# Kernel optimization log

Measured on AMD Instinct MI355X. Metric: run time of the kernel, lower is better.

Reference implementation:

```python
import jax, jax.numpy as jnp
import numpy as np

LN_EPS = 1e-5  # torch.nn.LayerNorm default


def setup_inputs() -> dict:
    key = jax.random.key(0)
    k1, k2 = jax.random.split(key)
    N, D_IN, D_OUT, G = 4096, 512, 512, 32
    x = jax.random.normal(k1, (N, D_IN), dtype=jnp.float32)
    ln_w = jnp.ones((D_IN,), dtype=jnp.float32)
    ln_b = jnp.zeros((D_IN,), dtype=jnp.float32)
    scale = 1.0 / (np.sqrt(D_IN) * np.sqrt(G))
    fouriercoeffs = jax.random.normal(k2, (2, D_OUT, D_IN, G), dtype=jnp.float32) * scale
    bias = jnp.zeros((1, D_OUT), dtype=jnp.float32)
    return {"x": x, "ln_w": ln_w, "ln_b": ln_b, "fouriercoeffs": fouriercoeffs, "bias": bias}


def reference(x, ln_w, ln_b, fouriercoeffs, bias):
    # LayerNorm over last dim
    mu = jnp.mean(x, axis=-1, keepdims=True)
    var = jnp.mean((x - mu) ** 2, axis=-1, keepdims=True)
    xn = (x - mu) * jax.lax.rsqrt(var + LN_EPS) * ln_w + ln_b
    G = fouriercoeffs.shape[-1]
    k = jnp.arange(1, G + 1, dtype=xn.dtype)           # [G]
    arg = xn[:, :, None] * k                            # [N, D_in, G]
    c = jnp.cos(arg)
    s = jnp.sin(arg)
    # contraction over (inputdim, gridsize) -> GEMM-shaped einsum
    y = jnp.einsum('big,oig->bo', c, fouriercoeffs[0])
    y = y + jnp.einsum('big,oig->bo', s, fouriercoeffs[1])
    y = y + bias
    return y
```

## Files before the change

### kernel.cpp

```cpp
#include <hip/hip_runtime.h>
#include <hip/hip_bf16.h>


#define N_ROWS 4096
#define D_IN   512
#define D_OUT  512
#define KT     16384
#define BM 128
#define BN 128
#define SPLITK 4

typedef short short8 __attribute__((ext_vector_type(8)));
typedef float float4v __attribute__((ext_vector_type(4)));

__device__ inline unsigned int pack2bf(float a, float b) {
    __hip_bfloat162 h = __float22bfloat162_rn(make_float2(a, b));
    union { __hip_bfloat162 h; unsigned int u; } cv;
    cv.h = h;
    return cv.u;
}

__device__ inline unsigned short bf16_1(float a) {
    union { float f; unsigned int u; } cv;
    cv.f = a;
    unsigned int r = (cv.u + 0x7fff + ((cv.u >> 16) & 1)) >> 16;
    return (unsigned short)r;
}

__global__ __launch_bounds__(256) void ln_stats(const float* __restrict__ x,
        float2* __restrict__ mu_rs) {
    const int t = threadIdx.x;
    const int row = blockIdx.x * 4 + (t >> 6);
    const int lane = t & 63;
    const float4* xr = (const float4*)(x + (size_t)row * D_IN);
    float4 a = xr[lane];
    float4 c = xr[lane + 64];
    float s = a.x + a.y + a.z + a.w + c.x + c.y + c.z + c.w;
    float q = a.x * a.x + a.y * a.y + a.z * a.z + a.w * a.w
            + c.x * c.x + c.y * c.y + c.z * c.z + c.w * c.w;
    #pragma unroll
    for (int off = 32; off > 0; off >>= 1) {
        s += __shfl_down(s, off, 64);
        q += __shfl_down(q, off, 64);
    }
    if (lane == 0) {
        float mu = s * (1.f / D_IN);
        float var = q * (1.f / D_IN) - mu * mu;
        mu_rs[row] = make_float2(mu, rsqrtf(var + 1e-5f));
    }
}

__global__ __launch_bounds__(256) void feat_seed(const float* __restrict__ x,
        const float* __restrict__ w, const float* __restrict__ b,
        const float2* __restrict__ mu_rs, float2* __restrict__ csT) {
    __shared__ float2 tile[64][65];
    const int t = threadIdx.x;
    const int r0 = blockIdx.x * 64, i0 = blockIdx.y * 64;
    const int rr = t >> 6;
    const int cc = t & 63;
    const float wv = w[i0 + cc], bv = b[i0 + cc];
    #pragma unroll
    for (int p = 0; p < 16; ++p) {
        const int row = r0 + p * 4 + rr;
        float v = x[(size_t)row * D_IN + i0 + cc];
        float2 mr = mu_rs[row];
        float xn = (v - mr.x) * mr.y * wv + bv;
        float sn, cn;
        __sincosf(xn, &sn, &cn);
        tile[p * 4 + rr][cc] = make_float2(cn, sn);
    }
    __syncthreads();
    #pragma unroll
    for (int p = 0; p < 16; ++p) {
        const int dim = p * 4 + rr;
        csT[(size_t)(i0 + dim) * N_ROWS + r0 + cc] = tile[cc][dim];
    }
}

__global__ __launch_bounds__(256) void cvt_kernel(const float* __restrict__ fc,
        unsigned short* __restrict__ Wb) {
    size_t e = ((size_t)blockIdx.x * 256 + threadIdx.x) * 8;
    const float4* in = (const float4*)(fc + e);
    float4 a = in[0];
    float4 c = in[1];
    uint4 o;
    o.x = pack2bf(a.x, a.y);
    o.y = pack2bf(a.z, a.w);
    o.z = pack2bf(c.x, c.y);
    o.w = pack2bf(c.z, c.w);
    *(uint4*)(Wb + e) = o;
}

__device__ inline void stage_feats(unsigned short* Abuf, float2 cs, int ttype,
                                   int frow, int ihalf) {
    const float c1 = cs.x, s1 = cs.y;
    const float c2 = c1 + c1;
    float prev = ttype ? 0.f : 1.f;
    float cur  = ttype ? s1 : c1;
    const int rbase = frow * 64;
    const int sw = frow & 7;
    unsigned int us[4];
    #pragma unroll
    for (int d = 0; d < 16; ++d) {
        float f0 = cur;
        float f1 = __builtin_fmaf(c2, cur, -prev);
        float f2 = __builtin_fmaf(c2, f1, -cur);
        prev = f1;
        cur = f2;
        us[d & 3] = pack2bf(f0, f1);
        if ((d & 3) == 3) {
            const int kc = ihalf * 4 + (d >> 2);
            *(uint4*)&Abuf[rbase + ((kc ^ sw) << 3)] =
                make_uint4(us[0], us[1], us[2], us[3]);
        }
    }
}

__device__ inline void gl_lds16(const unsigned short* gsrc, unsigned short* ldst) {
    __builtin_amdgcn_global_load_lds(
        (const __attribute__((address_space(1))) unsigned int*)gsrc,
        (__attribute__((address_space(3))) unsigned int*)ldst, 16, 0, 0);
}

__device__ inline void read_af(const unsigned short* As, short8 (&af)[2][4],
                               int wm, int lm, int lq, int swA) {
    #pragma unroll
    for (int h = 0; h < 2; ++h)
        #pragma unroll
        for (int tm = 0; tm < 4; ++tm)
            af[h][tm] = *(const short8*)
                &As[(wm + tm * 16 + lm) * 64 + (((h * 4 + lq) ^ swA) << 3)];
}

__device__ inline void read_bf(const unsigned short* Bp, short8 (&bf)[2][4],
                               int bBase) {
    #pragma unroll
    for (int h = 0; h < 2; ++h)
        #pragma unroll
        for (int tn = 0; tn < 4; ++tn)
            bf[h][tn] = *(const short8*)&Bp[bBase + tn * 1024 + h * 256];
}

__device__ inline void mfma_block(short8 (&af)[2][4], short8 (&bf)[2][4],
                                  float4v (&acc)[4][4]) {
    __builtin_amdgcn_s_setprio(1);
    #pragma unroll
    for (int h = 0; h < 2; ++h)
        #pragma unroll
        for (int tm = 0; tm < 4; ++tm)
            #pragma unroll
            for (int tn = 0; tn < 4; ++tn)
                acc[tm][tn] = __builtin_amdgcn_mfma_f32_16x16x32_bf16(
                    af[h][tm], bf[h][tn], acc[tm][tn], 0, 0, 0);
    __builtin_amdgcn_s_setprio(0);
}

__global__ __launch_bounds__(256, 2) void fkan_gemm(const float2* __restrict__ csT,
        const unsigned short* __restrict__ Wb, unsigned short* __restrict__ pb) {
    __shared__ unsigned short As[2][BM * 64];
    __shared__ unsigned short Bs[3][BN * 64];
    const int t = threadIdx.x;
    const int row0 = blockIdx.x * BM;
    const int col0 = blockIdx.y * BN;
    const int kz = blockIdx.z;
    const int k0 = kz * 4096;
    const int i0 = kz * 128;
    const int frow = t & 127;
    const int ihalf = t >> 7;
    const int l = t & 63, wv = t >> 6;
    const int wm = (wv & 1) * 64, wn = (wv >> 1) * 64;
    const int lm = l & 15, lq = l >> 4;
    const int c8 = l & 7, s8 = l >> 3;
    const unsigned short* Bg0 = Wb + (size_t)(col0 + wv * 32 + c8) * KT + k0 + s8 * 8;
    const int swA = lm & 7;
    const int bBase = ((wn >> 3) + (lm >> 3)) * 512 + lq * 64 + (lm & 7) * 8;

    const float2* csBase = csT + (size_t)(i0 + ihalf) * N_ROWS + row0 + frow;

    float4v acc[4][4];
    #pragma unroll
    for (int i = 0; i < 4; ++i)
        #pragma unroll
        for (int j = 0; j < 4; ++j)
            acc[i][j] = (float4v){0.f, 0.f, 0.f, 0.f};

    #pragma unroll
    for (int j = 0; j < 4; ++j)
        gl_lds16(Bg0 + (size_t)(j * 8) * KT, &Bs[0][(wv * 4 + j) * 512]);
    #pragma unroll
    for (int j = 0; j < 4; ++j)
        gl_lds16(Bg0 + 64 + (size_t)(j * 8) * KT, &Bs[1][(wv * 4 + j) * 512]);
    float2 c0 = csBase[0];
    float2 csA = csBase[2 * N_ROWS];
    stage_feats(&As[0][0], c0, 0, frow, ihalf);
    asm volatile("s_waitcnt vmcnt(4) lgkmcnt(0)" ::: "memory");
    __builtin_amdgcn_s_barrier();

    int rd = 0, wr = 2;
    for (int it = 0; it < 126; ++it) {
        const int p = it & 1;
        const unsigned short* Bp = &Bs[0][0] + rd * (BN * 64);
        {
            const int in = it + 2;
            const unsigned short* gb =
                Bg0 + (size_t)(in >> 6) * D_OUT * KT + (in & 63) * 64;
            unsigned short* ldst = &Bs[0][0] + wr * (BN * 64) + (wv * 4) * 512;
            #pragma unroll
            for (int j = 0; j < 4; ++j)
                gl_lds16(gb + (size_t)(j * 8) * KT, ldst + j * 512);
        }
        float2 csN = csBase[(size_t)(((it + 2) & 63) * 2) * N_ROWS];
        short8 af[2][4];
        read_af(&As[p][0], af, wm, lm, lq, swA);
        short8 bf[2][4];
        read_bf(Bp, bf, bBase);
        stage_feats(&As[p ^ 1][0], csA, (it + 1) >> 6, frow, ihalf);
        csA = csN;
        mfma_block(af, bf, acc);
        asm volatile("s_waitcnt vmcnt(5) lgkmcnt(0)" ::: "memory");
        __builtin_amdgcn_s_barrier();
        rd = (rd == 2) ? 0 : rd + 1;
        wr = (wr == 2) ? 0 : wr + 1;
    }
    {
        const unsigned short* Bp = &Bs[0][0];
        short8 af[2][4];
        read_af(&As[0][0], af, wm, lm, lq, swA);
        short8 bf[2][4];
        read_bf(Bp, bf, bBase);
        stage_feats(&As[1][0], csA, 1, frow, ihalf);
        mfma_block(af, bf, acc);
        asm volatile("s_waitcnt vmcnt(0) lgkmcnt(0)" ::: "memory");
        __builtin_amdgcn_s_barrier();
    }
    {
        const unsigned short* Bp = &Bs[1][0];
        short8 af[2][4];
        read_af(&As[1][0], af, wm, lm, lq, swA);
        short8 bf[2][4];
        read_bf(Bp, bf, bBase);
        mfma_block(af, bf, acc);
    }
    unsigned short* pc = pb + (size_t)kz * N_ROWS * D_OUT;
    #pragma unroll
    for (int tm = 0; tm < 4; ++tm)
        #pragma unroll
        for (int tn = 0; tn < 4; ++tn)
            #pragma unroll
            for (int r = 0; r < 4; ++r) {
                const int row = row0 + wm + tm * 16 + lq * 4 + r;
                const int col = col0 + wn + tn * 16 + lm;
                pc[(size_t)row * D_OUT + col] = bf16_1(acc[tm][tn][r]);
            }
}

__global__ __launch_bounds__(256) void reduce_kernel(const unsigned short* __restrict__ pb,
        const float* __restrict__ bias, float* __restrict__ out) {
    const size_t e = ((size_t)blockIdx.x * 256 + threadIdx.x) * 4;
    const int col = (int)(e & (D_OUT - 1));
    float4 s = *(const float4*)(bias + col);
    #pragma unroll
    for (int c = 0; c < SPLITK; ++c) {
        ushort4 u = *(const ushort4*)(pb + (size_t)c * N_ROWS * D_OUT + e);
        union { unsigned int u; float f; } f0, f1, f2, f3;
        f0.u = (unsigned int)u.x << 16;
        f1.u = (unsigned int)u.y << 16;
        f2.u = (unsigned int)u.z << 16;
        f3.u = (unsigned int)u.w << 16;
        s.x += f0.f; s.y += f1.f; s.z += f2.f; s.w += f3.f;
    }
    *(float4*)(out + e) = s;
}

extern "C" void kernel_launch(void* const* d_in, const int* in_sizes, int n_in,
                              void* d_out, int out_size, void* d_ws, size_t ws_size,
                              hipStream_t stream) {
    const float* x    = (const float*)d_in[0];
    const float* ln_w = (const float*)d_in[1];
    const float* ln_b = (const float*)d_in[2];
    const float* fc   = (const float*)d_in[3];
    const float* bias = (const float*)d_in[4];
    float* out = (float*)d_out;

    float2* csT = (float2*)d_ws;
    float2* mu_rs = (float2*)((char*)d_ws + (16u << 20));
    unsigned short* Wb = (unsigned short*)((char*)d_ws + (17u << 20));
    unsigned short* pbp = (unsigned short*)((char*)d_ws + (51u << 20));

    ln_stats<<<N_ROWS / 4, 256, 0, stream>>>(x, mu_rs);
    feat_seed<<<dim3(N_ROWS / 64, D_IN / 64), 256, 0, stream>>>(x, ln_w, ln_b, mu_rs, csT);
    cvt_kernel<<<8192, 256, 0, stream>>>(fc, Wb);
    fkan_gemm<<<dim3(N_ROWS / BM, D_OUT / BN, SPLITK), 256, 0, stream>>>(csT, Wb, pbp);
    reduce_kernel<<<2048, 256, 0, stream>>>(pbp, bias, out);
}
```

Before: 283.9 us.

## Generate Fourier A-fragments in registers and fuse preprocessing into one kernel

Merges the LayerNorm-stats, feature-seed and weight-conversion kernels into a single pre_kernel. That kernel also precomputes cos/sin at frequencies 1 and 16 as float4 seeds. The GEMM drops its A tile in LDS: each lane builds its bf16 A fragments directly in registers from the seeds with the Chebyshev recurrence, which removes LDS writes and reads and a barrier dependency. This adds per-lane recurrence work and duplicated seed loads from global, and the fused pre-kernel runs the weight conversion on only 256 blocks, which may lower its parallelism.

```diff
diff --git a/kernel.cpp b/kernel.cpp
--- a/kernel.cpp
+++ b/kernel.cpp
@@ -27,91 +27,66 @@
     return (unsigned short)r;
 }
 
-__global__ __launch_bounds__(256) void ln_stats(const float* __restrict__ x,
-        float2* __restrict__ mu_rs) {
+__global__ __launch_bounds__(256) void pre_kernel(const float* __restrict__ x,
+        const float* __restrict__ lnw, const float* __restrict__ lnb,
+        const float* __restrict__ fc, float4* __restrict__ csT2,
+        unsigned short* __restrict__ Wb) {
+    __shared__ __align__(16) float xs[16 * 516];
+    __shared__ float2 murs[16];
     const int t = threadIdx.x;
-    const int row = blockIdx.x * 4 + (t >> 6);
-    const int lane = t & 63;
-    const float4* xr = (const float4*)(x + (size_t)row * D_IN);
-    float4 a = xr[lane];
-    float4 c = xr[lane + 64];
-    float s = a.x + a.y + a.z + a.w + c.x + c.y + c.z + c.w;
-    float q = a.x * a.x + a.y * a.y + a.z * a.z + a.w * a.w
-            + c.x * c.x + c.y * c.y + c.z * c.z + c.w * c.w;
-    #pragma unroll
-    for (int off = 32; off > 0; off >>= 1) {
-        s += __shfl_down(s, off, 64);
-        q += __shfl_down(q, off, 64);
-    }
-    if (lane == 0) {
-        float mu = s * (1.f / D_IN);
-        float var = q * (1.f / D_IN) - mu * mu;
-        mu_rs[row] = make_float2(mu, rsqrtf(var + 1e-5f));
-    }
-}
-
-__global__ __launch_bounds__(256) void feat_seed(const float* __restrict__ x,
-        const float* __restrict__ w, const float* __restrict__ b,
-        const float2* __restrict__ mu_rs, float2* __restrict__ csT) {
-    __shared__ float2 tile[64][65];
-    const int t = threadIdx.x;
-    const int r0 = blockIdx.x * 64, i0 = blockIdx.y * 64;
-    const int rr = t >> 6;
-    const int cc = t & 63;
-    const float wv = w[i0 + cc], bv = b[i0 + cc];
-    #pragma unroll
-    for (int p = 0; p < 16; ++p) {
-        const int row = r0 + p * 4 + rr;
-        float v = x[(size_t)row * D_IN + i0 + cc];
-        float2 mr = mu_rs[row];
-        float xn = (v - mr.x) * mr.y * wv + bv;
-        float sn, cn;
-        __sincosf(xn, &sn, &cn);
-        tile[p * 4 + rr][cc] = make_float2(cn, sn);
+    const int r0 = blockIdx.x * 16;
+    {
+        const int row = t >> 4, tq = t & 15;
+        const float* xr = x + (size_t)(r0 + row) * D_IN;
+        float s = 0.f, q = 0.f;
+        #pragma unroll
+        for (int k = 0; k < 8; ++k) {
+            float4 v = *(const float4*)(xr + tq * 4 + k * 64);
+            *(float4*)&xs[row * 516 + tq * 4 + k * 64] = v;
+            s += v.x + v.y + v.z + v.w;
+            q += v.x * v.x + v.y * v.y + v.z * v.z + v.w * v.w;
+        }
+        #pragma unroll
+        for (int off = 8; off > 0; off >>= 1) {
+            s += __shfl_xor(s, off, 16);
+            q += __shfl_xor(q, off, 16);
+        }
+        if (tq == 0) {
+            float mu = s * (1.f / D_IN);
+            float var = q * (1.f / D_IN) - mu * mu;
+            murs[row] = make_float2(mu, rsqrtf(var + 1e-5f));
+        }
     }
     __syncthreads();
-    #pragma unroll
-    for (int p = 0; p < 16; ++p) {
-        const int dim = p * 4 + rr;
-        csT[(size_t)(i0 + dim) * N_ROWS + r0 + cc] = tile[cc][dim];
-    }
-}
-
-__global__ __launch_bounds__(256) void cvt_kernel(const float* __restrict__ fc,
-        unsigned short* __restrict__ Wb) {
-    size_t e = ((size_t)blockIdx.x * 256 + threadIdx.x) * 8;
-    const float4* in = (const float4*)(fc + e);
-    float4 a = in[0];
-    float4 c = in[1];
-    uint4 o;
-    o.x = pack2bf(a.x, a.y);
-    o.y = pack2bf(a.z, a.w);
-    o.z = pack2bf(c.x, c.y);
-    o.w = pack2bf(c.z, c.w);
-    *(uint4*)(Wb + e) = o;
-}
-
-__device__ inline void stage_feats(unsigned short* Abuf, float2 cs, int ttype,
-                                   int frow, int ihalf) {
-    const float c1 = cs.x, s1 = cs.y;
-    const float c2 = c1 + c1;
-    float prev = ttype ? 0.f : 1.f;
-    float cur  = ttype ? s1 : c1;
-    const int rbase = frow * 64;
-    const int sw = frow & 7;
-    unsigned int us[4];
-    #pragma unroll
-    for (int d = 0; d < 16; ++d) {
-        float f0 = cur;
-        float f1 = __builtin_fmaf(c2, cur, -prev);
-        float f2 = __builtin_fmaf(c2, f1, -cur);
-        prev = f1;
-        cur = f2;
-        us[d & 3] = pack2bf(f0, f1);
-        if ((d & 3) == 3) {
-            const int kc = ihalf * 4 + (d >> 2);
-            *(uint4*)&Abuf[rbase + ((kc ^ sw) << 3)] =
-                make_uint4(us[0], us[1], us[2], us[3]);
+    {
+        const int brow = t & 15, dimg = t >> 4;
+        const float2 mr = murs[brow];
+        #pragma unroll 4
+        for (int j = 0; j < 32; ++j) {
+            const int dim = j * 16 + dimg;
+            float xv = xs[brow * 516 + dim];
+            float xn = (xv - mr.x) * mr.y * lnw[dim] + lnb[dim];
+            float s1, c1;
+            __sincosf(xn, &s1, &c1);
+            float k2, c2, s2, c4, s4, c8, s8, c16, s16;
+            k2 = c1 + c1; c2  = __builtin_fmaf(k2, c1, -1.f); s2  = k2 * s1;
+            k2 = c2 + c2; c4  = __builtin_fmaf(k2, c2, -1.f); s4  = k2 * s2;
+            k2 = c4 + c4; c8  = __builtin_fmaf(k2, c4, -1.f); s8  = k2 * s4;
+            k2 = c8 + c8; c16 = __builtin_fmaf(k2, c8, -1.f); s16 = k2 * s8;
+            csT2[(size_t)dim * N_ROWS + r0 + brow] = make_float4(c1, s1, c16, s16);
+        }
+    }
+    {
+        size_t e = ((size_t)blockIdx.x * 256 + t) * 8;
+        for (int it2 = 0; it2 < 32; ++it2, e += (size_t)256 * 256 * 8) {
+            const float4* in = (const float4*)(fc + e);
+            float4 a = in[0], c = in[1];
+            uint4 o;
+            o.x = pack2bf(a.x, a.y);
+            o.y = pack2bf(a.z, a.w);
+            o.z = pack2bf(c.x, c.y);
+            o.w = pack2bf(c.z, c.w);
+            *(uint4*)(Wb + e) = o;
         }
     }
 }
@@ -122,42 +97,86 @@
         (__attribute__((address_space(3))) unsigned int*)ldst, 16, 0, 0);
 }
 
-__device__ inline void read_af(const unsigned short* As, short8 (&af)[2][4],
-                               int wm, int lm, int lq, int swA) {
-    #pragma unroll
-    for (int h = 0; h < 2; ++h)
+template<bool SIN>
+__device__ __forceinline__ void make_af(float4 sd, bool oddlq,
+                                        short8& a0, short8& a1) {
+    const float c1 = sd.x, s1 = sd.y, c16 = sd.z, s16 = sd.w;
+    const float k2 = c1 + c1;
+    float prev, cur;
+    if (SIN) {
+        float tt = s16 * c1;
+        float s17 = __builtin_fmaf(c16, s1, tt);
+        prev = oddlq ? s16 : 0.f;
+        cur  = oddlq ? s17 : s1;
+    } else {
+        float tt = s16 * s1;
+        float c17 = __builtin_fmaf(c16, c1, -tt);
+        prev = oddlq ? c16 : 1.f;
+        cur  = oddlq ? c17 : c1;
+    }
+    union { unsigned int u[8]; short8 s8v[2]; } U;
+    float p = prev, c = cur;
+    #pragma unroll
+    for (int d = 0; d < 8; ++d) {
+        float n1 = __builtin_fmaf(k2, c, -p);
+        U.u[d] = pack2bf(c, n1);
+        float n2 = __builtin_fmaf(k2, n1, -c);
+        p = n1;
+        c = n2;
+    }
+    a0 = U.s8v[0];
+    a1 = U.s8v[1];
+}
+
+template<bool SIN, bool PF, bool LDSEED>
+__device__ __forceinline__ void gemm_step(int it, int rd, int wr,
+        unsigned short (*Bs)[BN * 64], const unsigned short* Bg0, int wv,
+        const float4* const (&sb)[4], float4 (&sdU)[4], float4 (&sdL)[4],
+        int bBase, bool oddlq, float4v (&acc)[4][4]) {
+    if (PF) {
+        const int in = it + 2;
+        const unsigned short* gb =
+            Bg0 + (size_t)(in >> 6) * D_OUT * KT + (in & 63) * 64;
+        unsigned short* ldst = &Bs[wr][(wv * 4) * 512];
+        #pragma unroll
+        for (int j = 0; j < 4; ++j)
+            gl_lds16(gb + (size_t)(j * 8) * KT, ldst + j * 512);
+    }
+    if (LDSEED) {
         #pragma unroll
         for (int tm = 0; tm < 4; ++tm)
-            af[h][tm] = *(const short8*)
-                &As[(wm + tm * 16 + lm) * 64 + (((h * 4 + lq) ^ swA) << 3)];
-}
-
-__device__ inline void read_bf(const unsigned short* Bp, short8 (&bf)[2][4],
-                               int bBase) {
-    #pragma unroll
-    for (int h = 0; h < 2; ++h)
+            sdL[tm] = sb[tm][(size_t)((it + 1) & 63) * 8192];
+    }
+    const unsigned short* Bp = Bs[rd];
+    short8 bf0[4], bf1[4];
+    #pragma unroll
+    for (int tn = 0; tn < 4; ++tn) {
+        bf0[tn] = *(const short8*)&Bp[bBase + tn * 1024];
+        bf1[tn] = *(const short8*)&Bp[bBase + tn * 1024 + 64];
+    }
+    __builtin_amdgcn_s_setprio(1);
+    #pragma unroll
+    for (int tm = 0; tm < 4; ++tm) {
+        short8 a0, a1;
+        make_af<SIN>(sdU[tm], oddlq, a0, a1);
         #pragma unroll
         for (int tn = 0; tn < 4; ++tn)
-            bf[h][tn] = *(const short8*)&Bp[bBase + tn * 1024 + h * 256];
-}
-
-__device__ inline void mfma_block(short8 (&af)[2][4], short8 (&bf)[2][4],
-                                  float4v (&acc)[4][4]) {
-    __builtin_amdgcn_s_setprio(1);
-    #pragma unroll
-    for (int h = 0; h < 2; ++h)
-        #pragma unroll
-        for (int tm = 0; tm < 4; ++tm)
-            #pragma unroll
-            for (int tn = 0; tn < 4; ++tn)
-                acc[tm][tn] = __builtin_amdgcn_mfma_f32_16x16x32_bf16(
-                    af[h][tm], bf[h][tn], acc[tm][tn], 0, 0, 0);
+            acc[tm][tn] = __builtin_amdgcn_mfma_f32_16x16x32_bf16(
+                a0, bf0[tn], acc[tm][tn], 0, 0, 0);
+        #pragma unroll
+        for (int tn = 0; tn < 4; ++tn)
+            acc[tm][tn] = __builtin_amdgcn_mfma_f32_16x16x32_bf16(
+                a1, bf1[tn], acc[tm][tn], 0, 0, 0);
+    }
     __builtin_amdgcn_s_setprio(0);
 }
 
-__global__ __launch_bounds__(256, 2) void fkan_gemm(const float2* __restrict__ csT,
+#define FENCE8() do { asm volatile("s_waitcnt vmcnt(8)" ::: "memory"); \
+                      __builtin_amdgcn_s_barrier(); } while (0)
+#define ROT(v) (v) = ((v) == 2) ? 0 : (v) + 1
+
+__global__ __launch_bounds__(256, 2) void fkan_gemm(const float4* __restrict__ csT2,
         const unsigned short* __restrict__ Wb, unsigned short* __restrict__ pb) {
-    __shared__ unsigned short As[2][BM * 64];
     __shared__ unsigned short Bs[3][BN * 64];
     const int t = threadIdx.x;
     const int row0 = blockIdx.x * BM;
@@ -165,17 +184,19 @@
     const int kz = blockIdx.z;
     const int k0 = kz * 4096;
     const int i0 = kz * 128;
-    const int frow = t & 127;
-    const int ihalf = t >> 7;
     const int l = t & 63, wv = t >> 6;
     const int wm = (wv & 1) * 64, wn = (wv >> 1) * 64;
     const int lm = l & 15, lq = l >> 4;
+    const bool oddlq = (lq & 1) != 0;
     const int c8 = l & 7, s8 = l >> 3;
     const unsigned short* Bg0 = Wb + (size_t)(col0 + wv * 32 + c8) * KT + k0 + s8 * 8;
-    const int swA = lm & 7;
-    const int bBase = ((wn >> 3) + (lm >> 3)) * 512 + lq * 64 + (lm & 7) * 8;
-
-    const float2* csBase = csT + (size_t)(i0 + ihalf) * N_ROWS + row0 + frow;
+    const int bBase = ((wn >> 3) + (lm >> 3)) * 512
+                    + ((lq >> 1) * 4 + (lq & 1) * 2) * 64 + (lm & 7) * 8;
+    const float4* sb[4];
+    #pragma unroll
+    for (int tm = 0; tm < 4; ++tm)
+        sb[tm] = csT2 + (size_t)(i0 + (lq >> 1)) * N_ROWS
+               + (row0 + wm + tm * 16 + lm);
 
     float4v acc[4][4];
     #pragma unroll
@@ -184,63 +205,46 @@
         for (int j = 0; j < 4; ++j)
             acc[i][j] = (float4v){0.f, 0.f, 0.f, 0.f};
 
+    float4 sdA[4], sdB[4];
     #pragma unroll
     for (int j = 0; j < 4; ++j)
         gl_lds16(Bg0 + (size_t)(j * 8) * KT, &Bs[0][(wv * 4 + j) * 512]);
     #pragma unroll
     for (int j = 0; j < 4; ++j)
         gl_lds16(Bg0 + 64 + (size_t)(j * 8) * KT, &Bs[1][(wv * 4 + j) * 512]);
-    float2 c0 = csBase[0];
-    float2 csA = csBase[2 * N_ROWS];
-    stage_feats(&As[0][0], c0, 0, frow, ihalf);
-    asm volatile("s_waitcnt vmcnt(4) lgkmcnt(0)" ::: "memory");
+    #pragma unroll
+    for (int tm = 0; tm < 4; ++tm)
+        sdA[tm] = sb[tm][0];
+    asm volatile("s_waitcnt vmcnt(8)" ::: "memory");
     __builtin_amdgcn_s_barrier();
 
     int rd = 0, wr = 2;
-    for (int it = 0; it < 126; ++it) {
-        const int p = it & 1;
-        const unsigned short* Bp = &Bs[0][0] + rd * (BN * 64);
-        {
-            const int in = it + 2;
-            const unsigned short* gb =
-                Bg0 + (size_t)(in >> 6) * D_OUT * KT + (in & 63) * 64;
-            unsigned short* ldst = &Bs[0][0] + wr * (BN * 64) + (wv * 4) * 512;
-            #pragma unroll
-            for (int j = 0; j < 4; ++j)
-                gl_lds16(gb + (size_t)(j * 8) * KT, ldst + j * 512);
-        }
-        float2 csN = csBase[(size_t)(((it + 2) & 63) * 2) * N_ROWS];
-        short8 af[2][4];
-        read_af(&As[p][0], af, wm, lm, lq, swA);
-        short8 bf[2][4];
-        read_bf(Bp, bf, bBase);
-        stage_feats(&As[p ^ 1][0], csA, (it + 1) >> 6, frow, ihalf);
-        csA = csN;
-        mfma_block(af, bf, acc);
-        asm volatile("s_waitcnt vmcnt(5) lgkmcnt(0)" ::: "memory");
-        __builtin_amdgcn_s_barrier();
-        rd = (rd == 2) ? 0 : rd + 1;
-        wr = (wr == 2) ? 0 : wr + 1;
-    }
-    {
-        const unsigned short* Bp = &Bs[0][0];
-        short8 af[2][4];
-        read_af(&As[0][0], af, wm, lm, lq, swA);
-        short8 bf[2][4];
-        read_bf(Bp, bf, bBase);
-        stage_feats(&As[1][0], csA, 1, frow, ihalf);
-        mfma_block(af, bf, acc);
-        asm volatile("s_waitcnt vmcnt(0) lgkmcnt(0)" ::: "memory");
-        __builtin_amdgcn_s_barrier();
-    }
-    {
-        const unsigned short* Bp = &Bs[1][0];
-        short8 af[2][4];
-        read_af(&As[1][0], af, wm, lm, lq, swA);
-        short8 bf[2][4];
-        read_bf(Bp, bf, bBase);
-        mfma_block(af, bf, acc);
-    }
+    #pragma unroll 1
+    for (int it = 0; it < 64; it += 2) {
+        gemm_step<false, true, true>(it, rd, wr, Bs, Bg0, wv, sb, sdA, sdB,
+                                     bBase, oddlq, acc);
+        FENCE8(); ROT(rd); ROT(wr);
+        gemm_step<false, true, true>(it + 1, rd, wr, Bs, Bg0, wv, sb, sdB, sdA,
+                                     bBase, oddlq, acc);
+        FENCE8(); ROT(rd); ROT(wr);
+    }
+    #pragma unroll 1
+    for (int it = 64; it < 126; it += 2) {
+        gemm_step<true, true, true>(it, rd, wr, Bs, Bg0, wv, sb, sdA, sdB,
+                                    bBase, oddlq, acc);
+        FENCE8(); ROT(rd); ROT(wr);
+        gemm_step<true, true, true>(it + 1, rd, wr, Bs, Bg0, wv, sb, sdB, sdA,
+                                    bBase, oddlq, acc);
+        FENCE8(); ROT(rd); ROT(wr);
+    }
+    gemm_step<true, false, true>(126, rd, wr, Bs, Bg0, wv, sb, sdA, sdB,
+                                 bBase, oddlq, acc);
+    asm volatile("s_waitcnt vmcnt(4)" ::: "memory");
+    __builtin_amdgcn_s_barrier();
+    ROT(rd);
+    gemm_step<true, false, false>(127, rd, wr, Bs, Bg0, wv, sb, sdB, sdA,
+                                  bBase, oddlq, acc);
+
     unsigned short* pc = pb + (size_t)kz * N_ROWS * D_OUT;
     #pragma unroll
     for (int tm = 0; tm < 4; ++tm)
@@ -282,14 +286,11 @@
     const float* bias = (const float*)d_in[4];
     float* out = (float*)d_out;
 
-    float2* csT = (float2*)d_ws;
-    float2* mu_rs = (float2*)((char*)d_ws + (16u << 20));
-    unsigned short* Wb = (unsigned short*)((char*)d_ws + (17u << 20));
-    unsigned short* pbp = (unsigned short*)((char*)d_ws + (51u << 20));
-
-    ln_stats<<<N_ROWS / 4, 256, 0, stream>>>(x, mu_rs);
-    feat_seed<<<dim3(N_ROWS / 64, D_IN / 64), 256, 0, stream>>>(x, ln_w, ln_b, mu_rs, csT);
-    cvt_kernel<<<8192, 256, 0, stream>>>(fc, Wb);
-    fkan_gemm<<<dim3(N_ROWS / BM, D_OUT / BN, SPLITK), 256, 0, stream>>>(csT, Wb, pbp);
+    float4* csT2 = (float4*)d_ws;
+    unsigned short* Wb = (unsigned short*)((char*)d_ws + (32u << 20));
+    unsigned short* pbp = (unsigned short*)((char*)d_ws + (64u << 20));
+
+    pre_kernel<<<256, 256, 0, stream>>>(x, ln_w, ln_b, fc, csT2, Wb);
+    fkan_gemm<<<dim3(N_ROWS / BM, D_OUT / BN, SPLITK), 256, 0, stream>>>(csT2, Wb, pbp);
     reduce_kernel<<<2048, 256, 0, stream>>>(pbp, bias, out);
 }
```

New measurement: 332.2 us. +17.0%, slower.
